# Optimization experiments

Measured on AMD Instinct MI355X. Metric: run time of the kernel, lower is better.

## Reference

```python
import jax, jax.numpy as jnp
import numpy as np

N_NODES = 50000
N_EDGES = 800000
IN_CH = 256
HID = 256
NUM_GRAPHS = 512
LEAKY_SLOPE = 0.01
EPS = 1e-5


def gcn_conv(x, src, dst, W, b):
    # src/dst already include self loops. Symmetric normalization D^-1/2 A_hat D^-1/2.
    deg = jnp.zeros((N_NODES,), x.dtype).at[dst].add(1.0)
    dinv = jax.lax.rsqrt(deg)  # deg >= 1 because of self loops
    norm = dinv[src] * dinv[dst]  # [E+N]
    h = x @ W  # [N, H] dense GEMM
    agg = jnp.zeros((N_NODES, W.shape[1]), x.dtype).at[dst].add(h[src] * norm[:, None])
    return agg + b


def layer_norm(x, w, b):
    mu = jnp.mean(x, axis=-1, keepdims=True)
    var = jnp.mean(jnp.square(x - mu), axis=-1, keepdims=True)
    return (x - mu) * jax.lax.rsqrt(var + EPS) * w + b


def setup_inputs() -> dict:
    key = jax.random.key(0)
    ks = jax.random.split(key, 8)
    x = jax.random.normal(ks[0], (N_NODES, IN_CH), dtype=jnp.float32)
    edge_index = jax.random.randint(ks[1], (2, N_EDGES), 0, N_NODES, dtype=jnp.int64)
    batch = jnp.sort(jax.random.randint(ks[2], (N_NODES,), 0, NUM_GRAPHS, dtype=jnp.int64))
    s1 = (2.0 / IN_CH) ** 0.5
    s2 = (2.0 / HID) ** 0.5
    W1 = jax.random.normal(ks[3], (IN_CH, HID), dtype=jnp.float32) * s1
    b1 = jnp.zeros((HID,), jnp.float32)
    W2 = jax.random.normal(ks[4], (HID, HID), dtype=jnp.float32) * s2
    b2 = jnp.zeros((HID,), jnp.float32)
    ln1_w = jnp.ones((HID,), jnp.float32)
    ln1_b = jnp.zeros((HID,), jnp.float32)
    ln2_w = jnp.ones((HID,), jnp.float32)
    ln2_b = jnp.zeros((HID,), jnp.float32)
    return {"x": x, "edge_index": edge_index, "batch": batch,
            "W1": W1, "b1": b1, "ln1_w": ln1_w, "ln1_b": ln1_b,
            "W2": W2, "b2": b2, "ln2_w": ln2_w, "ln2_b": ln2_b}


def reference(x, edge_index, batch, W1, b1, ln1_w, ln1_b, W2, b2, ln2_w, ln2_b):
    loop = jnp.arange(N_NODES, dtype=edge_index.dtype)
    src = jnp.concatenate([edge_index[0], loop])
    dst = jnp.concatenate([edge_index[1], loop])

    h = gcn_conv(x, src, dst, W1, b1)
    h = layer_norm(h, ln1_w, ln1_b)
    h = jnp.where(h >= 0, h, LEAKY_SLOPE * h)

    h = gcn_conv(h, src, dst, W2, b2)
    h = layer_norm(h, ln2_w, ln2_b)
    h = jnp.where(h >= 0, h, LEAKY_SLOPE * h)

    # global mean pool per graph (dropout is inference no-op)
    sums = jax.ops.segment_sum(h, batch, num_segments=NUM_GRAPHS)
    cnts = jax.ops.segment_sum(jnp.ones((N_NODES,), h.dtype), batch, num_segments=NUM_GRAPHS)
    return sums / jnp.maximum(cnts, 1.0)[:, None]
```

## Files before the change

### kernel.cpp

```cpp
#include <hip/hip_runtime.h>

#define N_NODES 50000
#define N_EDGES 800000
#define CH 256
#define NUM_GRAPHS 512
#define LEAKY 0.01f
#define LN_EPS 1e-5f
#define NBLK ((N_NODES + 255) / 256)

typedef __attribute__((ext_vector_type(4))) float f32x4;
typedef __attribute__((ext_vector_type(2))) float f32x2;
typedef __attribute__((ext_vector_type(8))) short bf16x8;

__device__ __forceinline__ float b2f(unsigned short u) {
    union { unsigned int i; float f; } x; x.i = ((unsigned int)u) << 16; return x.f;
}
__device__ __forceinline__ unsigned short f2b(float f) {
    union { float f; unsigned int i; } x; x.f = f;
    unsigned int r = x.i + 0x7fffu + ((x.i >> 16) & 1u);
    return (unsigned short)(r >> 16);
}
__device__ __forceinline__ f32x2 b2f2(unsigned int u) {
    union { unsigned int i; float f; } lo, hi;
    lo.i = u << 16; hi.i = u & 0xffff0000u;
    f32x2 r; r.x = lo.f; r.y = hi.f; return r;
}
__device__ __forceinline__ unsigned int pack2(float a, float b) {
    return (unsigned int)f2b(a) | ((unsigned int)f2b(b) << 16);
}
__device__ __forceinline__ void gload16(const void* g, void* l) {
    __builtin_amdgcn_global_load_lds((const __attribute__((address_space(1))) unsigned int*)g,
                                     (__attribute__((address_space(3))) unsigned int*)l, 16, 0, 0);
}

__global__ void zero_ints(int* __restrict__ p, int n) {
    int i = blockIdx.x * blockDim.x + threadIdx.x;
    if (i < n) p[i] = 0;
}

__global__ void count_deg(const int* __restrict__ dst, int* __restrict__ cnt) {
    int e = blockIdx.x * blockDim.x + threadIdx.x;
    if (e < N_EDGES) atomicAdd(&cnt[dst[e]], 1);
}

__global__ __launch_bounds__(256) void block_reduce(const int* __restrict__ cnt,
                                                    int* __restrict__ bsum,
                                                    float* __restrict__ dinv) {
    __shared__ int s[256];
    int tid = threadIdx.x;
    int i = blockIdx.x * 256 + tid;
    int v = (i < N_NODES) ? cnt[i] : 0;
    if (i < N_NODES) dinv[i] = rsqrtf(1.0f + (float)v);
    s[tid] = v;
    __syncthreads();
    #pragma unroll
    for (int off = 128; off > 0; off >>= 1) {
        if (tid < off) s[tid] += s[tid + off];
        __syncthreads();
    }
    if (tid == 0) bsum[blockIdx.x] = s[0];
}

__global__ __launch_bounds__(256) void scan_bsums(int* __restrict__ bsum) {
    __shared__ int s[256];
    int tid = threadIdx.x;
    int v = (tid < NBLK) ? bsum[tid] : 0;
    s[tid] = v;
    __syncthreads();
    #pragma unroll
    for (int off = 1; off < 256; off <<= 1) {
        int t = (tid >= off) ? s[tid - off] : 0;
        __syncthreads();
        s[tid] += t;
        __syncthreads();
    }
    if (tid < NBLK) bsum[tid] = s[tid] - v;
}

__global__ __launch_bounds__(256) void block_scan(const int* __restrict__ cnt,
                                                  const int* __restrict__ bsum,
                                                  int* __restrict__ rowptr,
                                                  int* __restrict__ cursor) {
    __shared__ int s[256];
    int tid = threadIdx.x;
    int i = blockIdx.x * 256 + tid;
    int v = (i < N_NODES) ? cnt[i] : 0;
    s[tid] = v;
    __syncthreads();
    #pragma unroll
    for (int off = 1; off < 256; off <<= 1) {
        int t = (tid >= off) ? s[tid - off] : 0;
        __syncthreads();
        s[tid] += t;
        __syncthreads();
    }
    if (i < N_NODES) {
        int val = bsum[blockIdx.x] + s[tid] - v;
        rowptr[i] = val;
        cursor[i] = val;
        if (i == N_NODES - 1) rowptr[N_NODES] = bsum[blockIdx.x] + s[tid];
    }
}

__global__ void fill_csr(const int* __restrict__ src, const int* __restrict__ dst,
                         int* __restrict__ cursor, int* __restrict__ col) {
    int e = blockIdx.x * blockDim.x + threadIdx.x;
    if (e < N_EDGES) {
        int d = dst[e];
        int p = atomicAdd(&cursor[d], 1);
        col[p] = src[e];
    }
}

__global__ void transpose_w2(const float* __restrict__ W1f, const float* __restrict__ W2f,
                             unsigned short* __restrict__ WT1, unsigned short* __restrict__ WT2) {
    int k = blockIdx.x & 255;
    const float* W = (blockIdx.x >> 8) ? W2f : W1f;
    unsigned short* WT = (blockIdx.x >> 8) ? WT2 : WT1;
    int n = threadIdx.x;
    WT[n * CH + k] = f2b(W[k * CH + n]);
}

#define BM 128
#define BN 128
#define BK 64
#define SWZ(row, kb) (((row) * 128 + (kb) * 16) ^ (((row) & 7) << 4))

__global__ __launch_bounds__(256) void gemm_bf16(const unsigned short* __restrict__ A,
                                                 const unsigned short* __restrict__ BT,
                                                 const float* __restrict__ dinv,
                                                 unsigned short* __restrict__ out) {
    __shared__ unsigned short As[BM * BK];
    __shared__ unsigned short Bs[BN * BK];
    const int row0 = blockIdx.x * BM;
    const int col0 = blockIdx.y * BN;
    const int tid = threadIdx.x;
    const int w = tid >> 6, l = tid & 63;
    const int wr = w >> 1, wc = w & 1;
    const int lr = l & 15, lg = l >> 4;

    const int sr = l >> 3;
    const int kbp = l & 7;

    f32x4 acc[4][4] = {};

    for (int k0 = 0; k0 < CH; k0 += BK) {
        #pragma unroll
        for (int it = 0; it < 4; it++) {
            const int R = (w * 4 + it) * 8;
            const int r = R + sr;
            const int kb = kbp ^ (r & 7);
            gload16(&A[(size_t)(row0 + r) * CH + k0 + kb * 8], (char*)As + R * 128);
            gload16(&BT[(size_t)(col0 + r) * CH + k0 + kb * 8], (char*)Bs + R * 128);
        }
        __syncthreads();
        #pragma unroll
        for (int ks = 0; ks < 2; ks++) {
            bf16x8 af[4], bfr[4];
            #pragma unroll
            for (int fm = 0; fm < 4; fm++) {
                int r = wr * 64 + fm * 16 + lr;
                af[fm] = *(const bf16x8*)((const char*)As + SWZ(r, ks * 4 + lg));
            }
            #pragma unroll
            for (int fn = 0; fn < 4; fn++) {
                int r = wc * 64 + fn * 16 + lr;
                bfr[fn] = *(const bf16x8*)((const char*)Bs + SWZ(r, ks * 4 + lg));
            }
            #pragma unroll
            for (int fm = 0; fm < 4; fm++)
                #pragma unroll
                for (int fn = 0; fn < 4; fn++)
                    acc[fm][fn] = __builtin_amdgcn_mfma_f32_16x16x32_bf16(af[fm], bfr[fn], acc[fm][fn], 0, 0, 0);
        }
        __syncthreads();
    }
    #pragma unroll
    for (int fm = 0; fm < 4; fm++) {
        #pragma unroll
        for (int r = 0; r < 4; r++) {
            int grow = row0 + wr * 64 + fm * 16 + lg * 4 + r;
            if (grow < N_NODES) {
                float s = dinv[grow];
                #pragma unroll
                for (int fn = 0; fn < 4; fn++) {
                    int gcol = col0 + wc * 64 + fn * 16 + lr;
                    out[(size_t)grow * CH + gcol] = f2b(acc[fm][fn][r] * s);
                }
            }
        }
    }
}

__global__ __launch_bounds__(256) void gemm_f32a(const float* __restrict__ Af,
                                                 const unsigned short* __restrict__ BT,
                                                 const float* __restrict__ dinv,
                                                 unsigned short* __restrict__ out) {
    __shared__ unsigned short As[BM * BK];
    __shared__ unsigned short Bs[BN * BK];
    const int row0 = blockIdx.x * BM;
    const int col0 = blockIdx.y * BN;
    const int tid = threadIdx.x;
    const int w = tid >> 6, l = tid & 63;
    const int wr = w >> 1, wc = w & 1;
    const int lr = l & 15, lg = l >> 4;
    const int sr = l >> 3, kbp = l & 7;

    f32x4 acc[4][4] = {};

    for (int k0 = 0; k0 < CH; k0 += BK) {
        #pragma unroll
        for (int it = 0; it < 4; it++) {
            const int R = (w * 4 + it) * 8;
            const int r = R + sr;
            const int kb = kbp ^ (r & 7);
            gload16(&BT[(size_t)(col0 + r) * CH + k0 + kb * 8], (char*)Bs + R * 128);
        }
        #pragma unroll
        for (int it = 0; it < 4; it++) {
            int cidx = it * 256 + tid;
            int r = cidx >> 3, kb = cidx & 7;
            int grow = row0 + r;
            uint4 ua = make_uint4(0u, 0u, 0u, 0u);
            if (grow < N_NODES) {
                const float* ap = &Af[(size_t)grow * CH + k0 + kb * 8];
                float4 v0 = *(const float4*)ap;
                float4 v1 = *(const float4*)(ap + 4);
                ua = make_uint4(pack2(v0.x, v0.y), pack2(v0.z, v0.w),
                                pack2(v1.x, v1.y), pack2(v1.z, v1.w));
            }
            *(uint4*)((char*)As + SWZ(r, kb)) = ua;
        }
        __syncthreads();
        #pragma unroll
        for (int ks = 0; ks < 2; ks++) {
            bf16x8 af[4], bfr[4];
            #pragma unroll
            for (int fm = 0; fm < 4; fm++) {
                int r = wr * 64 + fm * 16 + lr;
                af[fm] = *(const bf16x8*)((const char*)As + SWZ(r, ks * 4 + lg));
            }
            #pragma unroll
            for (int fn = 0; fn < 4; fn++) {
                int r = wc * 64 + fn * 16 + lr;
                bfr[fn] = *(const bf16x8*)((const char*)Bs + SWZ(r, ks * 4 + lg));
            }
            #pragma unroll
            for (int fm = 0; fm < 4; fm++)
                #pragma unroll
                for (int fn = 0; fn < 4; fn++)
                    acc[fm][fn] = __builtin_amdgcn_mfma_f32_16x16x32_bf16(af[fm], bfr[fn], acc[fm][fn], 0, 0, 0);
        }
        __syncthreads();
    }
    #pragma unroll
    for (int fm = 0; fm < 4; fm++) {
        #pragma unroll
        for (int r = 0; r < 4; r++) {
            int grow = row0 + wr * 64 + fm * 16 + lg * 4 + r;
            if (grow < N_NODES) {
                float s = dinv[grow];
                #pragma unroll
                for (int fn = 0; fn < 4; fn++) {
                    int gcol = col0 + wc * 64 + fn * 16 + lr;
                    out[(size_t)grow * CH + gcol] = f2b(acc[fm][fn][r] * s);
                }
            }
        }
    }
}

__global__ __launch_bounds__(256) void agg_ln_bf16(const unsigned short* __restrict__ h,
                                                   const int* __restrict__ rowptr,
                                                   const int* __restrict__ col,
                                                   const float* __restrict__ dinv,
                                                   const float* __restrict__ bias,
                                                   const float* __restrict__ lnw,
                                                   const float* __restrict__ lnb,
                                                   unsigned short* __restrict__ out) {
    const int w = threadIdx.x >> 6, lane = threadIdx.x & 63;
    const int d = blockIdx.x * 4 + w;
    if (d >= N_NODES) return;
    const int c4 = lane * 4;
    const uint2* __restrict__ h2 = (const uint2*)h;

    f32x2 acc01, acc23;
    {
        uint2 u = h2[(unsigned)(d * 64 + lane)];
        acc01 = b2f2(u.x); acc23 = b2f2(u.y);
    }

    const int e0 = rowptr[d], e1 = rowptr[d + 1];
    for (int base = e0; base < e1; base += 64) {
        int nch = e1 - base; if (nch > 64) nch = 64;
        int cidx = (lane < nch) ? col[base + lane] : 0;
        int j = 0;
        for (; j + 8 <= nch; j += 8) {
            int s0 = __shfl(cidx, j),     s1 = __shfl(cidx, j + 1);
            int s2 = __shfl(cidx, j + 2), s3 = __shfl(cidx, j + 3);
            int s4 = __shfl(cidx, j + 4), s5 = __shfl(cidx, j + 5);
            int s6 = __shfl(cidx, j + 6), s7 = __shfl(cidx, j + 7);
            uint2 u0 = h2[(unsigned)(s0 * 64 + lane)];
            uint2 u1 = h2[(unsigned)(s1 * 64 + lane)];
            uint2 u2 = h2[(unsigned)(s2 * 64 + lane)];
            uint2 u3 = h2[(unsigned)(s3 * 64 + lane)];
            uint2 u4 = h2[(unsigned)(s4 * 64 + lane)];
            uint2 u5 = h2[(unsigned)(s5 * 64 + lane)];
            uint2 u6 = h2[(unsigned)(s6 * 64 + lane)];
            uint2 u7 = h2[(unsigned)(s7 * 64 + lane)];
            acc01 += b2f2(u0.x) + b2f2(u1.x) + b2f2(u2.x) + b2f2(u3.x);
            acc23 += b2f2(u0.y) + b2f2(u1.y) + b2f2(u2.y) + b2f2(u3.y);
            acc01 += b2f2(u4.x) + b2f2(u5.x) + b2f2(u6.x) + b2f2(u7.x);
            acc23 += b2f2(u4.y) + b2f2(u5.y) + b2f2(u6.y) + b2f2(u7.y);
        }
        for (; j + 4 <= nch; j += 4) {
            int s0 = __shfl(cidx, j),     s1 = __shfl(cidx, j + 1);
            int s2 = __shfl(cidx, j + 2), s3 = __shfl(cidx, j + 3);
            uint2 u0 = h2[(unsigned)(s0 * 64 + lane)];
            uint2 u1 = h2[(unsigned)(s1 * 64 + lane)];
            uint2 u2 = h2[(unsigned)(s2 * 64 + lane)];
            uint2 u3 = h2[(unsigned)(s3 * 64 + lane)];
            acc01 += b2f2(u0.x) + b2f2(u1.x) + b2f2(u2.x) + b2f2(u3.x);
            acc23 += b2f2(u0.y) + b2f2(u1.y) + b2f2(u2.y) + b2f2(u3.y);
        }
        for (; j < nch; j++) {
            int s = __shfl(cidx, j);
            uint2 u = h2[(unsigned)(s * 64 + lane)];
            acc01 += b2f2(u.x); acc23 += b2f2(u.y);
        }
    }
    float a0 = acc01.x, a1 = acc01.y, a2 = acc23.x, a3 = acc23.y;
    const float di = dinv[d];
    float4 bb = *(const float4*)&bias[c4];
    a0 = a0 * di + bb.x; a1 = a1 * di + bb.y; a2 = a2 * di + bb.z; a3 = a3 * di + bb.w;

    float s1 = a0 + a1 + a2 + a3;
    float s2 = a0 * a0 + a1 * a1 + a2 * a2 + a3 * a3;
    #pragma unroll
    for (int off = 32; off > 0; off >>= 1) {
        s1 += __shfl_xor(s1, off);
        s2 += __shfl_xor(s2, off);
    }
    const float mu = s1 * (1.0f / CH);
    const float rstd = rsqrtf(s2 * (1.0f / CH) - mu * mu + LN_EPS);
    float4 wv = *(const float4*)&lnw[c4];
    float4 bv = *(const float4*)&lnb[c4];
    float y0 = (a0 - mu) * rstd * wv.x + bv.x;
    float y1 = (a1 - mu) * rstd * wv.y + bv.y;
    float y2 = (a2 - mu) * rstd * wv.z + bv.z;
    float y3 = (a3 - mu) * rstd * wv.w + bv.w;
    y0 = (y0 >= 0.f) ? y0 : LEAKY * y0;
    y1 = (y1 >= 0.f) ? y1 : LEAKY * y1;
    y2 = (y2 >= 0.f) ? y2 : LEAKY * y2;
    y3 = (y3 >= 0.f) ? y3 : LEAKY * y3;
    *(ushort4*)&out[(size_t)d * CH + c4] = make_ushort4(f2b(y0), f2b(y1), f2b(y2), f2b(y3));
}

__global__ __launch_bounds__(256) void pool_mean_bf16(const unsigned short* __restrict__ feat,
                                                      const int* __restrict__ batch,
                                                      float* __restrict__ out) {
    const int g = blockIdx.x;
    const int w = threadIdx.x >> 6, lane = threadIdx.x & 63;
    int lo = 0, hi = N_NODES;
    while (lo < hi) { int mid = (lo + hi) >> 1; if (batch[mid] < g) lo = mid + 1; else hi = mid; }
    const int start = lo;
    hi = N_NODES;
    while (lo < hi) { int mid = (lo + hi) >> 1; if (batch[mid] < g + 1) lo = mid + 1; else hi = mid; }
    const int end = lo;

    float a0 = 0.f, a1 = 0.f, a2 = 0.f, a3 = 0.f;
    for (int n = start + w; n < end; n += 4) {
        ushort4 u = *(const ushort4*)&feat[(size_t)n * CH + lane * 4];
        a0 += b2f(u.x); a1 += b2f(u.y); a2 += b2f(u.z); a3 += b2f(u.w);
    }
    __shared__ float4 red[4][64];
    red[w][lane] = make_float4(a0, a1, a2, a3);
    __syncthreads();
    if (w == 0) {
        float4 t0 = red[0][lane], t1 = red[1][lane], t2 = red[2][lane], t3 = red[3][lane];
        const float inv = (end > start) ? 1.0f / (float)(end - start) : 0.0f;
        float4 o = make_float4((t0.x + t1.x + t2.x + t3.x) * inv,
                               (t0.y + t1.y + t2.y + t3.y) * inv,
                               (t0.z + t1.z + t2.z + t3.z) * inv,
                               (t0.w + t1.w + t2.w + t3.w) * inv);
        *(float4*)&out[(size_t)g * CH + lane * 4] = o;
    }
}

static inline size_t align256(size_t x) { return (x + 255) & ~(size_t)255; }

extern "C" void kernel_launch(void* const* d_in, const int* in_sizes, int n_in,
                              void* d_out, int out_size, void* d_ws, size_t ws_size,
                              hipStream_t stream) {
    const float* x    = (const float*)d_in[0];
    const int*   edge = (const int*)d_in[1];
    const int*   batch= (const int*)d_in[2];
    const float* W1   = (const float*)d_in[3];
    const float* b1   = (const float*)d_in[4];
    const float* ln1w = (const float*)d_in[5];
    const float* ln1b = (const float*)d_in[6];
    const float* W2   = (const float*)d_in[7];
    const float* b2   = (const float*)d_in[8];
    const float* ln2w = (const float*)d_in[9];
    const float* ln2b = (const float*)d_in[10];

    const int* src = edge;
    const int* dst = edge + N_EDGES;

    char* p = (char*)d_ws;
    int* cnt    = (int*)p;  p += align256(N_NODES * 4);
    int* cursor = (int*)p;  p += align256(N_NODES * 4);
    int* rowptr = (int*)p;  p += align256((N_NODES + 1) * 4);
    int* bsum   = (int*)p;  p += align256(NBLK * 4);
    float* dinv = (float*)p; p += align256(N_NODES * 4);
    int* col    = (int*)p;  p += align256(N_EDGES * 4);
    unsigned short* wt1 = (unsigned short*)p; p += align256(CH * CH * 2);
    unsigned short* wt2 = (unsigned short*)p; p += align256(CH * CH * 2);
    unsigned short* bufA = (unsigned short*)p; p += align256((size_t)N_NODES * CH * 2);
    unsigned short* bufB = (unsigned short*)p; p += align256((size_t)N_NODES * CH * 2);
    p += 32768;

    zero_ints<<<(N_NODES + 255) / 256, 256, 0, stream>>>(cnt, N_NODES);
    count_deg<<<(N_EDGES + 255) / 256, 256, 0, stream>>>(dst, cnt);
    block_reduce<<<NBLK, 256, 0, stream>>>(cnt, bsum, dinv);
    scan_bsums<<<1, 256, 0, stream>>>(bsum);
    block_scan<<<NBLK, 256, 0, stream>>>(cnt, bsum, rowptr, cursor);
    fill_csr<<<(N_EDGES + 255) / 256, 256, 0, stream>>>(src, dst, cursor, col);
    transpose_w2<<<2 * CH, CH, 0, stream>>>(W1, W2, wt1, wt2);

    dim3 ggrid((N_NODES + BM - 1) / BM, CH / BN);
    gemm_f32a<<<ggrid, 256, 0, stream>>>(x, wt1, dinv, bufA);
    agg_ln_bf16<<<(N_NODES + 3) / 4, 256, 0, stream>>>(bufA, rowptr, col, dinv, b1, ln1w, ln1b, bufB);
    gemm_bf16<<<ggrid, 256, 0, stream>>>(bufB, wt2, dinv, bufA);
    agg_ln_bf16<<<(N_NODES + 3) / 4, 256, 0, stream>>>(bufA, rowptr, col, dinv, b2, ln2w, ln2b, bufB);
    pool_mean_bf16<<<NUM_GRAPHS, 256, 0, stream>>>(bufB, batch, (float*)d_out);
}
```

Before: 293.0 us.

## Split aggregation into channel slices and defer LayerNorm into GEMM and pooling

The per-node aggregation kernel is replaced by a sliced gather: each wave handles one 32-channel slice, with lanes split across 8 edges, and writes raw pre-norm values plus partial sums. A separate small kernel finalizes the per-node mean and rstd. LayerNorm and LeakyReLU are then applied on the fly when the second GEMM loads its A tile and inside the pooling kernel, so no normalized intermediate is written. This aims at better memory-level parallelism in the gather, at the cost of more blocks, an extra stats buffer and kernel launch, and non-async A loads in the GEMM.

After: 505.7 us. 72.6% more time.

```diff
diff --git a/kernel.cpp b/kernel.cpp
--- a/kernel.cpp
+++ b/kernel.cpp
@@ -125,72 +125,6 @@
 #define BN 128
 #define BK 64
 #define SWZ(row, kb) (((row) * 128 + (kb) * 16) ^ (((row) & 7) << 4))
-
-__global__ __launch_bounds__(256) void gemm_bf16(const unsigned short* __restrict__ A,
-                                                 const unsigned short* __restrict__ BT,
-                                                 const float* __restrict__ dinv,
-                                                 unsigned short* __restrict__ out) {
-    __shared__ unsigned short As[BM * BK];
-    __shared__ unsigned short Bs[BN * BK];
-    const int row0 = blockIdx.x * BM;
-    const int col0 = blockIdx.y * BN;
-    const int tid = threadIdx.x;
-    const int w = tid >> 6, l = tid & 63;
-    const int wr = w >> 1, wc = w & 1;
-    const int lr = l & 15, lg = l >> 4;
-
-    const int sr = l >> 3;
-    const int kbp = l & 7;
-
-    f32x4 acc[4][4] = {};
-
-    for (int k0 = 0; k0 < CH; k0 += BK) {
-        #pragma unroll
-        for (int it = 0; it < 4; it++) {
-            const int R = (w * 4 + it) * 8;
-            const int r = R + sr;
-            const int kb = kbp ^ (r & 7);
-            gload16(&A[(size_t)(row0 + r) * CH + k0 + kb * 8], (char*)As + R * 128);
-            gload16(&BT[(size_t)(col0 + r) * CH + k0 + kb * 8], (char*)Bs + R * 128);
-        }
-        __syncthreads();
-        #pragma unroll
-        for (int ks = 0; ks < 2; ks++) {
-            bf16x8 af[4], bfr[4];
-            #pragma unroll
-            for (int fm = 0; fm < 4; fm++) {
-                int r = wr * 64 + fm * 16 + lr;
-                af[fm] = *(const bf16x8*)((const char*)As + SWZ(r, ks * 4 + lg));
-            }
-            #pragma unroll
-            for (int fn = 0; fn < 4; fn++) {
-                int r = wc * 64 + fn * 16 + lr;
-                bfr[fn] = *(const bf16x8*)((const char*)Bs + SWZ(r, ks * 4 + lg));
-            }
-            #pragma unroll
-            for (int fm = 0; fm < 4; fm++)
-                #pragma unroll
-                for (int fn = 0; fn < 4; fn++)
-                    acc[fm][fn] = __builtin_amdgcn_mfma_f32_16x16x32_bf16(af[fm], bfr[fn], acc[fm][fn], 0, 0, 0);
-        }
-        __syncthreads();
-    }
-    #pragma unroll
-    for (int fm = 0; fm < 4; fm++) {
-        #pragma unroll
-        for (int r = 0; r < 4; r++) {
-            int grow = row0 + wr * 64 + fm * 16 + lg * 4 + r;
-            if (grow < N_NODES) {
-                float s = dinv[grow];
-                #pragma unroll
-                for (int fn = 0; fn < 4; fn++) {
-                    int gcol = col0 + wc * 64 + fn * 16 + lr;
-                    out[(size_t)grow * CH + gcol] = f2b(acc[fm][fn][r] * s);
-                }
-            }
-        }
-    }
-}
 
 __global__ __launch_bounds__(256) void gemm_f32a(const float* __restrict__ Af,
                                                  const unsigned short* __restrict__ BT,
@@ -270,97 +204,186 @@
     }
 }
 
-__global__ __launch_bounds__(256) void agg_ln_bf16(const unsigned short* __restrict__ h,
-                                                   const int* __restrict__ rowptr,
-                                                   const int* __restrict__ col,
-                                                   const float* __restrict__ dinv,
-                                                   const float* __restrict__ bias,
-                                                   const float* __restrict__ lnw,
-                                                   const float* __restrict__ lnb,
-                                                   unsigned short* __restrict__ out) {
+__global__ __launch_bounds__(256) void gemm_ln_a(const unsigned short* __restrict__ raw,
+                                                 const float2* __restrict__ musig,
+                                                 const float* __restrict__ lnw,
+                                                 const float* __restrict__ lnb,
+                                                 const unsigned short* __restrict__ BT,
+                                                 const float* __restrict__ dinv,
+                                                 unsigned short* __restrict__ out) {
+    __shared__ unsigned short As[BM * BK];
+    __shared__ unsigned short Bs[BN * BK];
+    const int row0 = blockIdx.x * BM;
+    const int col0 = blockIdx.y * BN;
+    const int tid = threadIdx.x;
+    const int w = tid >> 6, l = tid & 63;
+    const int wr = w >> 1, wc = w & 1;
+    const int lr = l & 15, lg = l >> 4;
+    const int sr = l >> 3, kbp = l & 7;
+
+    f32x4 acc[4][4] = {};
+
+    for (int k0 = 0; k0 < CH; k0 += BK) {
+        #pragma unroll
+        for (int it = 0; it < 4; it++) {
+            const int R = (w * 4 + it) * 8;
+            const int r = R + sr;
+            const int kb = kbp ^ (r & 7);
+            gload16(&BT[(size_t)(col0 + r) * CH + k0 + kb * 8], (char*)Bs + R * 128);
+        }
+        #pragma unroll
+        for (int it = 0; it < 4; it++) {
+            int cidx = it * 256 + tid;
+            int r = cidx >> 3, kb = cidx & 7;
+            int grow = row0 + r;
+            uint4 ua = make_uint4(0u, 0u, 0u, 0u);
+            if (grow < N_NODES) {
+                uint4 u = ((const uint4*)raw)[(size_t)grow * 32 + (k0 >> 3) + kb];
+                float2 ms = musig[grow];
+                float4 w0 = ((const float4*)lnw)[(k0 >> 2) + kb * 2];
+                float4 w1 = ((const float4*)lnw)[(k0 >> 2) + kb * 2 + 1];
+                float4 b0 = ((const float4*)lnb)[(k0 >> 2) + kb * 2];
+                float4 b1 = ((const float4*)lnb)[(k0 >> 2) + kb * 2 + 1];
+                f32x2 v0 = b2f2(u.x), v1 = b2f2(u.y), v2 = b2f2(u.z), v3 = b2f2(u.w);
+                float y0 = (v0.x - ms.x) * ms.y * w0.x + b0.x;
+                float y1 = (v0.y - ms.x) * ms.y * w0.y + b0.y;
+                float y2 = (v1.x - ms.x) * ms.y * w0.z + b0.z;
+                float y3 = (v1.y - ms.x) * ms.y * w0.w + b0.w;
+                float y4 = (v2.x - ms.x) * ms.y * w1.x + b1.x;
+                float y5 = (v2.y - ms.x) * ms.y * w1.y + b1.y;
+                float y6 = (v3.x - ms.x) * ms.y * w1.z + b1.z;
+                float y7 = (v3.y - ms.x) * ms.y * w1.w + b1.w;
+                y0 = fmaxf(y0, LEAKY * y0); y1 = fmaxf(y1, LEAKY * y1);
+                y2 = fmaxf(y2, LEAKY * y2); y3 = fmaxf(y3, LEAKY * y3);
+                y4 = fmaxf(y4, LEAKY * y4); y5 = fmaxf(y5, LEAKY * y5);
+                y6 = fmaxf(y6, LEAKY * y6); y7 = fmaxf(y7, LEAKY * y7);
+                ua = make_uint4(pack2(y0, y1), pack2(y2, y3), pack2(y4, y5), pack2(y6, y7));
+            }
+            *(uint4*)((char*)As + SWZ(r, kb)) = ua;
+        }
+        __syncthreads();
+        #pragma unroll
+        for (int ks = 0; ks < 2; ks++) {
+            bf16x8 af[4], bfr[4];
+            #pragma unroll
+            for (int fm = 0; fm < 4; fm++) {
+                int r = wr * 64 + fm * 16 + lr;
+                af[fm] = *(const bf16x8*)((const char*)As + SWZ(r, ks * 4 + lg));
+            }
+            #pragma unroll
+            for (int fn = 0; fn < 4; fn++) {
+                int r = wc * 64 + fn * 16 + lr;
+                bfr[fn] = *(const bf16x8*)((const char*)Bs + SWZ(r, ks * 4 + lg));
+            }
+            #pragma unroll
+            for (int fm = 0; fm < 4; fm++)
+                #pragma unroll
+                for (int fn = 0; fn < 4; fn++)
+                    acc[fm][fn] = __builtin_amdgcn_mfma_f32_16x16x32_bf16(af[fm], bfr[fn], acc[fm][fn], 0, 0, 0);
+        }
+        __syncthreads();
+    }
+    #pragma unroll
+    for (int fm = 0; fm < 4; fm++) {
+        #pragma unroll
+        for (int r = 0; r < 4; r++) {
+            int grow = row0 + wr * 64 + fm * 16 + lg * 4 + r;
+            if (grow < N_NODES) {
+                float s = dinv[grow];
+                #pragma unroll
+                for (int fn = 0; fn < 4; fn++) {
+                    int gcol = col0 + wc * 64 + fn * 16 + lr;
+                    out[(size_t)grow * CH + gcol] = f2b(acc[fm][fn][r] * s);
+                }
+            }
+        }
+    }
+}
+
+__global__ __launch_bounds__(256) void gather_slice(const unsigned short* __restrict__ h,
+                                                    const int* __restrict__ rowptr,
+                                                    const int* __restrict__ col,
+                                                    const float* __restrict__ dinv,
+                                                    const float* __restrict__ bias,
+                                                    unsigned short* __restrict__ raw,
+                                                    float* __restrict__ stats) {
     const int w = threadIdx.x >> 6, lane = threadIdx.x & 63;
-    const int d = blockIdx.x * 4 + w;
-    if (d >= N_NODES) return;
-    const int c4 = lane * 4;
+    const unsigned b = blockIdx.x;
+    const int slice = b & 7;
+    const int d = (int)(b >> 3) * 4 + w;
+    const int c = lane & 7, es = lane >> 3;
+    const int du2 = slice * 8 + c;
     const uint2* __restrict__ h2 = (const uint2*)h;
 
-    f32x2 acc01, acc23;
-    {
-        uint2 u = h2[(unsigned)(d * 64 + lane)];
+    f32x2 acc01 = {0.f, 0.f}, acc23 = {0.f, 0.f};
+    if (es == 0) {
+        uint2 u = h2[(size_t)d * 64 + du2];
         acc01 = b2f2(u.x); acc23 = b2f2(u.y);
     }
 
     const int e0 = rowptr[d], e1 = rowptr[d + 1];
     for (int base = e0; base < e1; base += 64) {
-        int nch = e1 - base; if (nch > 64) nch = 64;
-        int cidx = (lane < nch) ? col[base + lane] : 0;
-        int j = 0;
-        for (; j + 8 <= nch; j += 8) {
-            int s0 = __shfl(cidx, j),     s1 = __shfl(cidx, j + 1);
-            int s2 = __shfl(cidx, j + 2), s3 = __shfl(cidx, j + 3);
-            int s4 = __shfl(cidx, j + 4), s5 = __shfl(cidx, j + 5);
-            int s6 = __shfl(cidx, j + 6), s7 = __shfl(cidx, j + 7);
-            uint2 u0 = h2[(unsigned)(s0 * 64 + lane)];
-            uint2 u1 = h2[(unsigned)(s1 * 64 + lane)];
-            uint2 u2 = h2[(unsigned)(s2 * 64 + lane)];
-            uint2 u3 = h2[(unsigned)(s3 * 64 + lane)];
-            uint2 u4 = h2[(unsigned)(s4 * 64 + lane)];
-            uint2 u5 = h2[(unsigned)(s5 * 64 + lane)];
-            uint2 u6 = h2[(unsigned)(s6 * 64 + lane)];
-            uint2 u7 = h2[(unsigned)(s7 * 64 + lane)];
-            acc01 += b2f2(u0.x) + b2f2(u1.x) + b2f2(u2.x) + b2f2(u3.x);
-            acc23 += b2f2(u0.y) + b2f2(u1.y) + b2f2(u2.y) + b2f2(u3.y);
-            acc01 += b2f2(u4.x) + b2f2(u5.x) + b2f2(u6.x) + b2f2(u7.x);
-            acc23 += b2f2(u4.y) + b2f2(u5.y) + b2f2(u6.y) + b2f2(u7.y);
-        }
-        for (; j + 4 <= nch; j += 4) {
-            int s0 = __shfl(cidx, j),     s1 = __shfl(cidx, j + 1);
-            int s2 = __shfl(cidx, j + 2), s3 = __shfl(cidx, j + 3);
-            uint2 u0 = h2[(unsigned)(s0 * 64 + lane)];
-            uint2 u1 = h2[(unsigned)(s1 * 64 + lane)];
-            uint2 u2 = h2[(unsigned)(s2 * 64 + lane)];
-            uint2 u3 = h2[(unsigned)(s3 * 64 + lane)];
-            acc01 += b2f2(u0.x) + b2f2(u1.x) + b2f2(u2.x) + b2f2(u3.x);
-            acc23 += b2f2(u0.y) + b2f2(u1.y) + b2f2(u2.y) + b2f2(u3.y);
-        }
-        for (; j < nch; j++) {
-            int s = __shfl(cidx, j);
-            uint2 u = h2[(unsigned)(s * 64 + lane)];
+        int n = e1 - base; if (n > 64) n = 64;
+        int cidx = (lane < n) ? col[base + lane] : 0;
+        const int full = n >> 3;
+        for (int j = 0; j < full; j++) {
+            int s = __shfl(cidx, j * 8 + es);
+            uint2 u = h2[(size_t)s * 64 + du2];
             acc01 += b2f2(u.x); acc23 += b2f2(u.y);
         }
-    }
-    float a0 = acc01.x, a1 = acc01.y, a2 = acc23.x, a3 = acc23.y;
+        const int rem = n & 7;
+        if (rem) {
+            int s = __shfl(cidx, full * 8 + (es < rem ? es : 0));
+            if (es < rem) {
+                uint2 u = h2[(size_t)s * 64 + du2];
+                acc01 += b2f2(u.x); acc23 += b2f2(u.y);
+            }
+        }
+    }
+    #pragma unroll
+    for (int off = 8; off < 64; off <<= 1) {
+        acc01.x += __shfl_xor(acc01.x, off); acc01.y += __shfl_xor(acc01.y, off);
+        acc23.x += __shfl_xor(acc23.x, off); acc23.y += __shfl_xor(acc23.y, off);
+    }
     const float di = dinv[d];
-    float4 bb = *(const float4*)&bias[c4];
-    a0 = a0 * di + bb.x; a1 = a1 * di + bb.y; a2 = a2 * di + bb.z; a3 = a3 * di + bb.w;
-
+    float4 bb = ((const float4*)bias)[slice * 8 + c];
+    float a0 = acc01.x * di + bb.x, a1 = acc01.y * di + bb.y;
+    float a2 = acc23.x * di + bb.z, a3 = acc23.y * di + bb.w;
     float s1 = a0 + a1 + a2 + a3;
     float s2 = a0 * a0 + a1 * a1 + a2 * a2 + a3 * a3;
     #pragma unroll
-    for (int off = 32; off > 0; off >>= 1) {
-        s1 += __shfl_xor(s1, off);
-        s2 += __shfl_xor(s2, off);
-    }
-    const float mu = s1 * (1.0f / CH);
-    const float rstd = rsqrtf(s2 * (1.0f / CH) - mu * mu + LN_EPS);
-    float4 wv = *(const float4*)&lnw[c4];
-    float4 bv = *(const float4*)&lnb[c4];
-    float y0 = (a0 - mu) * rstd * wv.x + bv.x;
-    float y1 = (a1 - mu) * rstd * wv.y + bv.y;
-    float y2 = (a2 - mu) * rstd * wv.z + bv.z;
-    float y3 = (a3 - mu) * rstd * wv.w + bv.w;
-    y0 = (y0 >= 0.f) ? y0 : LEAKY * y0;
-    y1 = (y1 >= 0.f) ? y1 : LEAKY * y1;
-    y2 = (y2 >= 0.f) ? y2 : LEAKY * y2;
-    y3 = (y3 >= 0.f) ? y3 : LEAKY * y3;
-    *(ushort4*)&out[(size_t)d * CH + c4] = make_ushort4(f2b(y0), f2b(y1), f2b(y2), f2b(y3));
-}
-
-__global__ __launch_bounds__(256) void pool_mean_bf16(const unsigned short* __restrict__ feat,
-                                                      const int* __restrict__ batch,
-                                                      float* __restrict__ out) {
+    for (int off = 1; off < 8; off <<= 1) {
+        s1 += __shfl_xor(s1, off); s2 += __shfl_xor(s2, off);
+    }
+    if (lane == 0) {
+        stats[d * 16 + slice * 2]     = s1;
+        stats[d * 16 + slice * 2 + 1] = s2;
+    }
+    if (es == 0)
+        ((uint2*)raw)[(size_t)d * 64 + du2] = make_uint2(pack2(a0, a1), pack2(a2, a3));
+}
+
+__global__ void finalize_stats(const float* __restrict__ stats, float2* __restrict__ musig) {
+    int d = blockIdx.x * 256 + threadIdx.x;
+    if (d < N_NODES) {
+        float s1 = 0.f, s2 = 0.f;
+        #pragma unroll
+        for (int i = 0; i < 8; i++) { s1 += stats[d * 16 + i * 2]; s2 += stats[d * 16 + i * 2 + 1]; }
+        float mu = s1 * (1.0f / CH);
+        float var = s2 * (1.0f / CH) - mu * mu;
+        musig[d] = make_float2(mu, rsqrtf(var + LN_EPS));
+    }
+}
+
+__global__ __launch_bounds__(256) void pool_ln(const unsigned short* __restrict__ raw,
+                                               const float2* __restrict__ musig,
+                                               const float* __restrict__ lnw,
+                                               const float* __restrict__ lnb,
+                                               const int* __restrict__ batch,
+                                               float* __restrict__ out) {
     const int g = blockIdx.x;
     const int w = threadIdx.x >> 6, lane = threadIdx.x & 63;
+    const int c4 = lane * 4;
     int lo = 0, hi = N_NODES;
     while (lo < hi) { int mid = (lo + hi) >> 1; if (batch[mid] < g) lo = mid + 1; else hi = mid; }
     const int start = lo;
@@ -368,10 +391,21 @@
     while (lo < hi) { int mid = (lo + hi) >> 1; if (batch[mid] < g + 1) lo = mid + 1; else hi = mid; }
     const int end = lo;
 
+    float4 wv = *(const float4*)&lnw[c4];
+    float4 bv = *(const float4*)&lnb[c4];
     float a0 = 0.f, a1 = 0.f, a2 = 0.f, a3 = 0.f;
     for (int n = start + w; n < end; n += 4) {
-        ushort4 u = *(const ushort4*)&feat[(size_t)n * CH + lane * 4];
-        a0 += b2f(u.x); a1 += b2f(u.y); a2 += b2f(u.z); a3 += b2f(u.w);
+        uint2 u = ((const uint2*)raw)[(size_t)n * 64 + lane];
+        f32x2 r01 = b2f2(u.x), r23 = b2f2(u.y);
+        float2 ms = musig[n];
+        float y0 = (r01.x - ms.x) * ms.y * wv.x + bv.x;
+        float y1 = (r01.y - ms.x) * ms.y * wv.y + bv.y;
+        float y2 = (r23.x - ms.x) * ms.y * wv.z + bv.z;
+        float y3 = (r23.y - ms.x) * ms.y * wv.w + bv.w;
+        a0 += fmaxf(y0, LEAKY * y0);
+        a1 += fmaxf(y1, LEAKY * y1);
+        a2 += fmaxf(y2, LEAKY * y2);
+        a3 += fmaxf(y3, LEAKY * y3);
     }
     __shared__ float4 red[4][64];
     red[w][lane] = make_float4(a0, a1, a2, a3);
@@ -413,11 +447,13 @@
     int* rowptr = (int*)p;  p += align256((N_NODES + 1) * 4);
     int* bsum   = (int*)p;  p += align256(NBLK * 4);
     float* dinv = (float*)p; p += align256(N_NODES * 4);
+    float* stats= (float*)p; p += align256((size_t)N_NODES * 16 * 4);
+    float2* musig=(float2*)p; p += align256((size_t)N_NODES * 8);
     int* col    = (int*)p;  p += align256(N_EDGES * 4);
     unsigned short* wt1 = (unsigned short*)p; p += align256(CH * CH * 2);
     unsigned short* wt2 = (unsigned short*)p; p += align256(CH * CH * 2);
-    unsigned short* bufA = (unsigned short*)p; p += align256((size_t)N_NODES * CH * 2);
-    unsigned short* bufB = (unsigned short*)p; p += align256((size_t)N_NODES * CH * 2);
+    unsigned short* bufH = (unsigned short*)p; p += align256((size_t)N_NODES * CH * 2);
+    unsigned short* bufR = (unsigned short*)p; p += align256((size_t)N_NODES * CH * 2);
     p += 32768;
 
     zero_ints<<<(N_NODES + 255) / 256, 256, 0, stream>>>(cnt, N_NODES);
@@ -426,12 +462,16 @@
     scan_bsums<<<1, 256, 0, stream>>>(bsum);
     block_scan<<<NBLK, 256, 0, stream>>>(cnt, bsum, rowptr, cursor);
     fill_csr<<<(N_EDGES + 255) / 256, 256, 0, stream>>>(src, dst, cursor, col);
-    transpose_w2<<<2 * CH, CH, 0, stream>>>(W1, W2, wt1, wt2);
+    transpose_w2<<<2 * CH, 256, 0, stream>>>(W1, W2, wt1, wt2);
 
     dim3 ggrid((N_NODES + BM - 1) / BM, CH / BN);
-    gemm_f32a<<<ggrid, 256, 0, stream>>>(x, wt1, dinv, bufA);
-    agg_ln_bf16<<<(N_NODES + 3) / 4, 256, 0, stream>>>(bufA, rowptr, col, dinv, b1, ln1w, ln1b, bufB);
-    gemm_bf16<<<ggrid, 256, 0, stream>>>(bufB, wt2, dinv, bufA);
-    agg_ln_bf16<<<(N_NODES + 3) / 4, 256, 0, stream>>>(bufA, rowptr, col, dinv, b2, ln2w, ln2b, bufB);
-    pool_mean_bf16<<<NUM_GRAPHS, 256, 0, stream>>>(bufB, batch, (float*)d_out);
-}
+    const int sblocks = (N_NODES / 4) * 8;
+
+    gemm_f32a<<<ggrid, 256, 0, stream>>>(x, wt1, dinv, bufH);
+    gather_slice<<<sblocks, 256, 0, stream>>>(bufH, rowptr, col, dinv, b1, bufR, stats);
+    finalize_stats<<<(N_NODES + 255) / 256, 256, 0, stream>>>(stats, musig);
+    gemm_ln_a<<<ggrid, 256, 0, stream>>>(bufR, musig, ln1w, ln1b, wt2, dinv, bufH);
+    gather_slice<<<sblocks, 256, 0, stream>>>(bufH, rowptr, col, dinv, b2, bufR, stats);
+    finalize_stats<<<(N_NODES + 255) / 256, 256, 0, stream>>>(stats, musig);
+    pool_ln<<<NUM_GRAPHS, 256, 0, stream>>>(bufR, musig, ln2w, ln2b, batch, (float*)d_out);
+}
```

## Gather two edges per wavefront with 16-byte loads and fold block-sum scan

Applied to the files above, without the earlier changes.

The aggregation kernel now splits each 64-lane wavefront into two half-waves. Each half processes alternate neighbours, loading 8 bf16 channels per lane with 16-byte loads, and the halves are combined with a cross-half shuffle before LayerNorm. This doubles the number of neighbour rows in flight per instruction and widens memory transactions in the latency-bound gather, at the cost of an extra reduction step and idle lanes on the store. Separately, the single-block scan of block sums is folded into block_scan, where every block redundantly rescans the block totals, removing one kernel launch.

Measured after the change: 292.4 us. Within noise of the previous version (-0.2%).

```diff
diff --git a/kernel.cpp b/kernel.cpp
--- a/kernel.cpp
+++ b/kernel.cpp
@@ -61,29 +61,24 @@
     if (tid == 0) bsum[blockIdx.x] = s[0];
 }
 
-__global__ __launch_bounds__(256) void scan_bsums(int* __restrict__ bsum) {
-    __shared__ int s[256];
-    int tid = threadIdx.x;
-    int v = (tid < NBLK) ? bsum[tid] : 0;
-    s[tid] = v;
-    __syncthreads();
-    #pragma unroll
-    for (int off = 1; off < 256; off <<= 1) {
-        int t = (tid >= off) ? s[tid - off] : 0;
-        __syncthreads();
-        s[tid] += t;
-        __syncthreads();
-    }
-    if (tid < NBLK) bsum[tid] = s[tid] - v;
-}
-
 __global__ __launch_bounds__(256) void block_scan(const int* __restrict__ cnt,
                                                   const int* __restrict__ bsum,
                                                   int* __restrict__ rowptr,
                                                   int* __restrict__ cursor) {
-    __shared__ int s[256];
+    __shared__ int s[256], sb[256];
     int tid = threadIdx.x;
     int i = blockIdx.x * 256 + tid;
+    int bv = (tid < NBLK) ? bsum[tid] : 0;
+    sb[tid] = bv;
+    __syncthreads();
+    #pragma unroll
+    for (int off = 1; off < 256; off <<= 1) {
+        int t = (tid >= off) ? sb[tid - off] : 0;
+        __syncthreads();
+        sb[tid] += t;
+        __syncthreads();
+    }
+    const int base = (blockIdx.x == 0) ? 0 : sb[blockIdx.x - 1];
     int v = (i < N_NODES) ? cnt[i] : 0;
     s[tid] = v;
     __syncthreads();
@@ -95,10 +90,10 @@
         __syncthreads();
     }
     if (i < N_NODES) {
-        int val = bsum[blockIdx.x] + s[tid] - v;
+        int val = base + s[tid] - v;
         rowptr[i] = val;
         cursor[i] = val;
-        if (i == N_NODES - 1) rowptr[N_NODES] = bsum[blockIdx.x] + s[tid];
+        if (i == N_NODES - 1) rowptr[N_NODES] = base + s[tid];
     }
 }
 
@@ -138,9 +133,7 @@
     const int w = tid >> 6, l = tid & 63;
     const int wr = w >> 1, wc = w & 1;
     const int lr = l & 15, lg = l >> 4;
-
-    const int sr = l >> 3;
-    const int kbp = l & 7;
+    const int sr = l >> 3, kbp = l & 7;
 
     f32x4 acc[4][4] = {};
 
@@ -281,79 +274,90 @@
     const int w = threadIdx.x >> 6, lane = threadIdx.x & 63;
     const int d = blockIdx.x * 4 + w;
     if (d >= N_NODES) return;
-    const int c4 = lane * 4;
-    const uint2* __restrict__ h2 = (const uint2*)h;
-
-    f32x2 acc01, acc23;
-    {
-        uint2 u = h2[(unsigned)(d * 64 + lane)];
-        acc01 = b2f2(u.x); acc23 = b2f2(u.y);
+    const int c = lane & 31, es = lane >> 5;
+    const uint4* __restrict__ h4 = (const uint4*)h;
+
+    f32x2 a01 = {0.f, 0.f}, a23 = {0.f, 0.f}, a45 = {0.f, 0.f}, a67 = {0.f, 0.f};
+    if (es == 0) {
+        uint4 u = h4[(size_t)d * 32 + c];
+        a01 = b2f2(u.x); a23 = b2f2(u.y); a45 = b2f2(u.z); a67 = b2f2(u.w);
     }
 
     const int e0 = rowptr[d], e1 = rowptr[d + 1];
     for (int base = e0; base < e1; base += 64) {
-        int nch = e1 - base; if (nch > 64) nch = 64;
-        int cidx = (lane < nch) ? col[base + lane] : 0;
+        int n = e1 - base; if (n > 64) n = 64;
+        int cidx = (lane < n) ? col[base + lane] : 0;
+        const int pairs = n >> 1;
         int j = 0;
-        for (; j + 8 <= nch; j += 8) {
-            int s0 = __shfl(cidx, j),     s1 = __shfl(cidx, j + 1);
-            int s2 = __shfl(cidx, j + 2), s3 = __shfl(cidx, j + 3);
-            int s4 = __shfl(cidx, j + 4), s5 = __shfl(cidx, j + 5);
-            int s6 = __shfl(cidx, j + 6), s7 = __shfl(cidx, j + 7);
-            uint2 u0 = h2[(unsigned)(s0 * 64 + lane)];
-            uint2 u1 = h2[(unsigned)(s1 * 64 + lane)];
-            uint2 u2 = h2[(unsigned)(s2 * 64 + lane)];
-            uint2 u3 = h2[(unsigned)(s3 * 64 + lane)];
-            uint2 u4 = h2[(unsigned)(s4 * 64 + lane)];
-            uint2 u5 = h2[(unsigned)(s5 * 64 + lane)];
-            uint2 u6 = h2[(unsigned)(s6 * 64 + lane)];
-            uint2 u7 = h2[(unsigned)(s7 * 64 + lane)];
-            acc01 += b2f2(u0.x) + b2f2(u1.x) + b2f2(u2.x) + b2f2(u3.x);
-            acc23 += b2f2(u0.y) + b2f2(u1.y) + b2f2(u2.y) + b2f2(u3.y);
-            acc01 += b2f2(u4.x) + b2f2(u5.x) + b2f2(u6.x) + b2f2(u7.x);
-            acc23 += b2f2(u4.y) + b2f2(u5.y) + b2f2(u6.y) + b2f2(u7.y);
-        }
-        for (; j + 4 <= nch; j += 4) {
-            int s0 = __shfl(cidx, j),     s1 = __shfl(cidx, j + 1);
-            int s2 = __shfl(cidx, j + 2), s3 = __shfl(cidx, j + 3);
-            uint2 u0 = h2[(unsigned)(s0 * 64 + lane)];
-            uint2 u1 = h2[(unsigned)(s1 * 64 + lane)];
-            uint2 u2 = h2[(unsigned)(s2 * 64 + lane)];
-            uint2 u3 = h2[(unsigned)(s3 * 64 + lane)];
-            acc01 += b2f2(u0.x) + b2f2(u1.x) + b2f2(u2.x) + b2f2(u3.x);
-            acc23 += b2f2(u0.y) + b2f2(u1.y) + b2f2(u2.y) + b2f2(u3.y);
-        }
-        for (; j < nch; j++) {
-            int s = __shfl(cidx, j);
-            uint2 u = h2[(unsigned)(s * 64 + lane)];
-            acc01 += b2f2(u.x); acc23 += b2f2(u.y);
-        }
-    }
-    float a0 = acc01.x, a1 = acc01.y, a2 = acc23.x, a3 = acc23.y;
+        for (; j + 4 <= pairs; j += 4) {
+            int s0 = __shfl(cidx, (j + 0) * 2 + es);
+            int s1 = __shfl(cidx, (j + 1) * 2 + es);
+            int s2 = __shfl(cidx, (j + 2) * 2 + es);
+            int s3 = __shfl(cidx, (j + 3) * 2 + es);
+            uint4 u0 = h4[(size_t)s0 * 32 + c];
+            uint4 u1 = h4[(size_t)s1 * 32 + c];
+            uint4 u2 = h4[(size_t)s2 * 32 + c];
+            uint4 u3 = h4[(size_t)s3 * 32 + c];
+            a01 += b2f2(u0.x) + b2f2(u1.x) + b2f2(u2.x) + b2f2(u3.x);
+            a23 += b2f2(u0.y) + b2f2(u1.y) + b2f2(u2.y) + b2f2(u3.y);
+            a45 += b2f2(u0.z) + b2f2(u1.z) + b2f2(u2.z) + b2f2(u3.z);
+            a67 += b2f2(u0.w) + b2f2(u1.w) + b2f2(u2.w) + b2f2(u3.w);
+        }
+        for (; j < pairs; j++) {
+            int s = __shfl(cidx, j * 2 + es);
+            uint4 u = h4[(size_t)s * 32 + c];
+            a01 += b2f2(u.x); a23 += b2f2(u.y); a45 += b2f2(u.z); a67 += b2f2(u.w);
+        }
+        if (n & 1) {
+            int s = __shfl(cidx, n - 1);
+            if (es == 0) {
+                uint4 u = h4[(size_t)s * 32 + c];
+                a01 += b2f2(u.x); a23 += b2f2(u.y); a45 += b2f2(u.z); a67 += b2f2(u.w);
+            }
+        }
+    }
+    a01.x += __shfl_xor(a01.x, 32); a01.y += __shfl_xor(a01.y, 32);
+    a23.x += __shfl_xor(a23.x, 32); a23.y += __shfl_xor(a23.y, 32);
+    a45.x += __shfl_xor(a45.x, 32); a45.y += __shfl_xor(a45.y, 32);
+    a67.x += __shfl_xor(a67.x, 32); a67.y += __shfl_xor(a67.y, 32);
+
     const float di = dinv[d];
-    float4 bb = *(const float4*)&bias[c4];
-    a0 = a0 * di + bb.x; a1 = a1 * di + bb.y; a2 = a2 * di + bb.z; a3 = a3 * di + bb.w;
-
-    float s1 = a0 + a1 + a2 + a3;
-    float s2 = a0 * a0 + a1 * a1 + a2 * a2 + a3 * a3;
-    #pragma unroll
-    for (int off = 32; off > 0; off >>= 1) {
+    float4 bb0 = ((const float4*)bias)[c * 2];
+    float4 bb1 = ((const float4*)bias)[c * 2 + 1];
+    float x0 = a01.x * di + bb0.x, x1 = a01.y * di + bb0.y;
+    float x2 = a23.x * di + bb0.z, x3 = a23.y * di + bb0.w;
+    float x4 = a45.x * di + bb1.x, x5 = a45.y * di + bb1.y;
+    float x6 = a67.x * di + bb1.z, x7 = a67.y * di + bb1.w;
+
+    float s1 = x0 + x1 + x2 + x3 + x4 + x5 + x6 + x7;
+    float s2 = x0 * x0 + x1 * x1 + x2 * x2 + x3 * x3 + x4 * x4 + x5 * x5 + x6 * x6 + x7 * x7;
+    #pragma unroll
+    for (int off = 1; off < 32; off <<= 1) {
         s1 += __shfl_xor(s1, off);
         s2 += __shfl_xor(s2, off);
     }
     const float mu = s1 * (1.0f / CH);
     const float rstd = rsqrtf(s2 * (1.0f / CH) - mu * mu + LN_EPS);
-    float4 wv = *(const float4*)&lnw[c4];
-    float4 bv = *(const float4*)&lnb[c4];
-    float y0 = (a0 - mu) * rstd * wv.x + bv.x;
-    float y1 = (a1 - mu) * rstd * wv.y + bv.y;
-    float y2 = (a2 - mu) * rstd * wv.z + bv.z;
-    float y3 = (a3 - mu) * rstd * wv.w + bv.w;
-    y0 = (y0 >= 0.f) ? y0 : LEAKY * y0;
-    y1 = (y1 >= 0.f) ? y1 : LEAKY * y1;
-    y2 = (y2 >= 0.f) ? y2 : LEAKY * y2;
-    y3 = (y3 >= 0.f) ? y3 : LEAKY * y3;
-    *(ushort4*)&out[(size_t)d * CH + c4] = make_ushort4(f2b(y0), f2b(y1), f2b(y2), f2b(y3));
+    float4 w0 = ((const float4*)lnw)[c * 2];
+    float4 w1 = ((const float4*)lnw)[c * 2 + 1];
+    float4 b0 = ((const float4*)lnb)[c * 2];
+    float4 b1 = ((const float4*)lnb)[c * 2 + 1];
+    float y0 = (x0 - mu) * rstd * w0.x + b0.x;
+    float y1 = (x1 - mu) * rstd * w0.y + b0.y;
+    float y2 = (x2 - mu) * rstd * w0.z + b0.z;
+    float y3 = (x3 - mu) * rstd * w0.w + b0.w;
+    float y4 = (x4 - mu) * rstd * w1.x + b1.x;
+    float y5 = (x5 - mu) * rstd * w1.y + b1.y;
+    float y6 = (x6 - mu) * rstd * w1.z + b1.z;
+    float y7 = (x7 - mu) * rstd * w1.w + b1.w;
+    y0 = fmaxf(y0, LEAKY * y0); y1 = fmaxf(y1, LEAKY * y1);
+    y2 = fmaxf(y2, LEAKY * y2); y3 = fmaxf(y3, LEAKY * y3);
+    y4 = fmaxf(y4, LEAKY * y4); y5 = fmaxf(y5, LEAKY * y5);
+    y6 = fmaxf(y6, LEAKY * y6); y7 = fmaxf(y7, LEAKY * y7);
+    if (es == 0) {
+        uint4 o = make_uint4(pack2(y0, y1), pack2(y2, y3), pack2(y4, y5), pack2(y6, y7));
+        ((uint4*)out)[(size_t)d * 32 + c] = o;
+    }
 }
 
 __global__ __launch_bounds__(256) void pool_mean_bf16(const unsigned short* __restrict__ feat,
@@ -423,10 +427,9 @@
     zero_ints<<<(N_NODES + 255) / 256, 256, 0, stream>>>(cnt, N_NODES);
     count_deg<<<(N_EDGES + 255) / 256, 256, 0, stream>>>(dst, cnt);
     block_reduce<<<NBLK, 256, 0, stream>>>(cnt, bsum, dinv);
-    scan_bsums<<<1, 256, 0, stream>>>(bsum);
     block_scan<<<NBLK, 256, 0, stream>>>(cnt, bsum, rowptr, cursor);
     fill_csr<<<(N_EDGES + 255) / 256, 256, 0, stream>>>(src, dst, cursor, col);
-    transpose_w2<<<2 * CH, CH, 0, stream>>>(W1, W2, wt1, wt2);
+    transpose_w2<<<2 * CH, 256, 0, stream>>>(W1, W2, wt1, wt2);
 
     dim3 ggrid((N_NODES + BM - 1) / BM, CH / BN);
     gemm_f32a<<<ggrid, 256, 0, stream>>>(x, wt1, dinv, bufA);
```
